# Performance work log

Hardware: AMD Instinct MI355X
Metric: run time of the kernel (lower is better)

Reference implementation:

```python
import jax, jax.numpy as jnp
import numpy as np

EPS_COMBINE = 1e-6   # F.normalize eps in embedder
EPS_FINAL = 1e-12    # F.normalize default eps


def _l2norm(x, eps):
    # torch F.normalize: x / max(||x||_2, eps)
    n = jnp.sqrt(jnp.sum(x * x, axis=-1, keepdims=True))
    return x / jnp.maximum(n, eps)


def setup_inputs() -> dict:
    key = jax.random.key(0)
    ks = jax.random.split(key, 6)
    B, H, E = 16384, 768, 8
    s1 = 1.0 / np.sqrt(H)
    s2 = 1.0 / np.sqrt(H // 2)
    return {
        "embedding": jax.random.normal(ks[0], (B, H), jnp.float32),
        "gate_logits": jax.random.normal(ks[1], (B, E), jnp.float32),
        "W1": jax.random.normal(ks[2], (E, H, H // 2), jnp.float32) * s1,
        "b1": jax.random.normal(ks[3], (E, H // 2), jnp.float32) * s1,
        "W2": jax.random.normal(ks[4], (E, H // 2, H), jnp.float32) * s2,
        "b2": jax.random.normal(ks[5], (E, H), jnp.float32) * s2,
    }


def reference(embedding, gate_logits, W1, b1, W2, b2):
    # cls(): softmax + top-1 mask (sbmoe_top1)
    p = jax.nn.softmax(gate_logits, axis=-1)               # [B, E]
    mask = jax.nn.one_hot(jnp.argmax(p, axis=-1), p.shape[-1], dtype=p.dtype)
    gate = p * mask                                        # [B, E]

    # embedder(): run EVERY expert (2-layer MLP) on all samples
    h = jax.nn.relu(jnp.einsum('bd,edh->beh', embedding, W1) + b1[None])  # [B, E, H/2]
    embs = jnp.einsum('beh,ehd->bed', h, W2) + b2[None]                   # [B, E, H]

    # weighted combine + normalize + residual
    combined = jnp.einsum('bed,be->bd', embs, gate)        # [B, H]
    out = _l2norm(combined, EPS_COMBINE) + embedding
    # normalize=True
    return _l2norm(out, EPS_FINAL)
```

## Files before the change

### kernel.cpp

```cpp
#include <hip/hip_runtime.h>
#include <hip/hip_bf16.h>
#include <stdint.h>

#define B_N   16384
#define H_DIM 768
#define HH    384
#define NE    8
#define CSTRIDE 32

typedef __attribute__((ext_vector_type(8))) short bf16x8;
typedef __attribute__((ext_vector_type(4))) float f32x4;

__device__ __forceinline__ unsigned short f2bf(float f) {
    uint32_t u = __float_as_uint(f);
    return (unsigned short)((u + 0x7fffu + ((u >> 16) & 1u)) >> 16);
}

__global__ void zero_counts_kernel(int* __restrict__ counts) {
    if (threadIdx.x < NE) counts[threadIdx.x * CSTRIDE] = 0;
}

__global__ void route_kernel(const float* __restrict__ logits,
                             int* __restrict__ counts,
                             int* __restrict__ buckets) {
    __shared__ int lcnt[NE];
    __shared__ int lbase[NE];
    const int tid = threadIdx.x;
    if (tid < NE) lcnt[tid] = 0;
    __syncthreads();

    const int b = blockIdx.x * 256 + tid;
    const float* l = logits + (size_t)b * NE;
    float best = l[0];
    int be = 0;
#pragma unroll
    for (int e = 1; e < NE; ++e) {
        float v = l[e];
        if (v > best) { best = v; be = e; }
    }
    const int lpos = atomicAdd(&lcnt[be], 1);
    __syncthreads();
    if (tid < NE) lbase[tid] = atomicAdd(&counts[tid * CSTRIDE], lcnt[tid]);
    __syncthreads();
    buckets[be * B_N + lbase[be] + lpos] = b;
}

__global__ void transpose_cvt_kernel(const float* __restrict__ W1,
                                     const float* __restrict__ W2,
                                     unsigned short* __restrict__ W1T,
                                     unsigned short* __restrict__ W2T,
                                     int* __restrict__ counts) {
    if (blockIdx.x == 0 && blockIdx.y == 0 && blockIdx.z == 0 && threadIdx.x < NE)
        counts[threadIdx.x * CSTRIDE] = 0;

    const int z = blockIdx.z;
    const int R = z ? HH : H_DIM;
    const int C = z ? H_DIM : HH;
    const float* src = (z ? W2 : W1) + (size_t)blockIdx.y * R * C;
    unsigned short* dst = (z ? W2T : W1T) + (size_t)blockIdx.y * R * C;

    const int ctiles = C >> 5;
    const int ty = blockIdx.x / ctiles;
    const int tx = blockIdx.x % ctiles;

    __shared__ float Ts[32][33];
    const int lr = threadIdx.x >> 3;
    const int lc = (threadIdx.x & 7) * 4;

    f32x4 v = *reinterpret_cast<const f32x4*>(src + (size_t)(ty * 32 + lr) * C + tx * 32 + lc);
    Ts[lr][lc + 0] = v[0]; Ts[lr][lc + 1] = v[1];
    Ts[lr][lc + 2] = v[2]; Ts[lr][lc + 3] = v[3];
    __syncthreads();

    ushort4 o;
    o.x = f2bf(Ts[lc + 0][lr]);
    o.y = f2bf(Ts[lc + 1][lr]);
    o.z = f2bf(Ts[lc + 2][lr]);
    o.w = f2bf(Ts[lc + 3][lr]);
    *reinterpret_cast<ushort4*>(dst + (size_t)(tx * 32 + lr) * R + ty * 32 + lc) = o;
}

template<int KTOT, int NTOT, bool A_F32, bool RELU, bool OUTBF>
__global__ __launch_bounds__(512, 6)
void gemm_kernel(const void* __restrict__ Aglob,
                 const unsigned short* __restrict__ WT,
                 const float* __restrict__ bias,
                 const int* __restrict__ counts,
                 const int* __restrict__ buckets,
                 void* __restrict__ Cout) {
    __shared__ __align__(16) unsigned char AsB[2][64 * 128];
    __shared__ __align__(16) unsigned char BsB[2][128 * 128];
    __shared__ int sidx[64];

    const int wgid   = blockIdx.x;
    const int e      = wgid & 7;
    const int rest   = wgid >> 3;
    const int mtile  = rest & 255;
    const int nchunk = rest >> 8;
    const int cnt    = counts[e * CSTRIDE];
    const int base   = mtile * 64;
    if (base >= cnt) return;
    const int ns  = min(64, cnt - base);
    const int tid = threadIdx.x;

    if (tid < 64) sidx[tid] = buckets[e * B_N + base + (tid < ns ? tid : 0)];
    __syncthreads();

    const int ar = tid >> 3, aq = tid & 7;
    const int bn = tid >> 2, bq = tid & 3;
    const float*          arow_f = nullptr;
    const unsigned short* arow_h = nullptr;
    if (A_F32) arow_f = (const float*)Aglob + (size_t)sidx[ar] * KTOT + aq * 8;
    else       arow_h = (const unsigned short*)Aglob + (size_t)sidx[ar] * KTOT + aq * 8;
    const unsigned short* brow =
        WT + ((size_t)e * NTOT + nchunk * 128 + bn) * KTOT + bq * 16;

    const int a_slot  = (ar << 7) + ((aq * 16) ^ ((ar & 7) << 4));
    const int b_slot0 = (bn << 7) + (((bq * 32)     ) ^ ((bn & 7) << 4));
    const int b_slot1 = (bn << 7) + (((bq * 32) + 16) ^ ((bn & 7) << 4));

    const int w = tid >> 6, lane = tid & 63;
    const int wr = w >> 2, wc = w & 3;
    const int fr = lane & 15, fq = lane >> 4;

    f32x4 acc[2][2];
#pragma unroll
    for (int mi = 0; mi < 2; ++mi)
#pragma unroll
        for (int ni = 0; ni < 2; ++ni) acc[mi][ni] = (f32x4)(0.f);

    bf16x8 aReg;
    f32x4  bReg0, bReg1;

    auto LOAD = [&](int k0) {
        if (A_F32) {
            f32x4 f0 = *reinterpret_cast<const f32x4*>(arow_f + k0);
            f32x4 f1 = *reinterpret_cast<const f32x4*>(arow_f + k0 + 4);
            bf16x8 p;
#pragma unroll
            for (int i = 0; i < 4; ++i) {
                p[i]     = (short)f2bf(f0[i]);
                p[i + 4] = (short)f2bf(f1[i]);
            }
            aReg = p;
        } else {
            aReg = *reinterpret_cast<const bf16x8*>(arow_h + k0);
        }
        bReg0 = *reinterpret_cast<const f32x4*>(brow + k0);
        bReg1 = *reinterpret_cast<const f32x4*>(brow + k0 + 8);
    };
    auto WRITE = [&](int buf) {
        *reinterpret_cast<bf16x8*>(&AsB[buf][a_slot])  = aReg;
        *reinterpret_cast<f32x4*>(&BsB[buf][b_slot0]) = bReg0;
        *reinterpret_cast<f32x4*>(&BsB[buf][b_slot1]) = bReg1;
    };
    auto COMPUTE = [&](int buf) {
#pragma unroll
        for (int s = 0; s < 2; ++s) {
            const int kb = s * 64 + fq * 16;
            bf16x8 af[2], bfr[2];
#pragma unroll
            for (int mi = 0; mi < 2; ++mi) {
                int row = wr * 32 + mi * 16 + fr;
                af[mi] = *reinterpret_cast<const bf16x8*>(
                    &AsB[buf][(row << 7) + (kb ^ ((row & 7) << 4))]);
            }
#pragma unroll
            for (int ni = 0; ni < 2; ++ni) {
                int row = wc * 32 + ni * 16 + fr;
                bfr[ni] = *reinterpret_cast<const bf16x8*>(
                    &BsB[buf][(row << 7) + (kb ^ ((row & 7) << 4))]);
            }
#pragma unroll
            for (int mi = 0; mi < 2; ++mi)
#pragma unroll
                for (int ni = 0; ni < 2; ++ni)
                    acc[mi][ni] = __builtin_amdgcn_mfma_f32_16x16x32_bf16(
                        af[mi], bfr[ni], acc[mi][ni], 0, 0, 0);
        }
    };

    LOAD(0);
    WRITE(0);
    __syncthreads();
    int cur = 0;
    for (int k0 = 64; k0 < KTOT; k0 += 64) {
        LOAD(k0);
        COMPUTE(cur);
        WRITE(cur ^ 1);
        __syncthreads();
        cur ^= 1;
    }
    COMPUTE(cur);

    const float* be = bias + (size_t)e * NTOT + nchunk * 128 + wc * 32;
#pragma unroll
    for (int mi = 0; mi < 2; ++mi) {
        const int rl0 = wr * 32 + mi * 16 + fq * 4;
#pragma unroll
        for (int ni = 0; ni < 2; ++ni) {
            const int coll = ni * 16 + fr;
            const int colg = nchunk * 128 + wc * 32 + coll;
            const float bb = be[coll];
#pragma unroll
            for (int r2 = 0; r2 < 4; ++r2) {
                const int rl = rl0 + r2;
                if (rl < ns) {
                    float v = acc[mi][ni][r2] + bb;
                    if (RELU) v = fmaxf(v, 0.f);
                    size_t o = (size_t)sidx[rl] * NTOT + colg;
                    if (OUTBF) ((unsigned short*)Cout)[o] = f2bf(v);
                    else       ((float*)Cout)[o] = v;
                }
            }
        }
    }
}

template<bool YB>
__global__ void norm_kernel(const float* __restrict__ emb,
                            const unsigned short* __restrict__ y2b,
                            float* __restrict__ out) {
    const int row  = blockIdx.x * 4 + (threadIdx.x >> 6);
    const int lane = threadIdx.x & 63;
    const float* x = emb + (size_t)row * H_DIM;
    float* o = out + (size_t)row * H_DIM;

    float s1 = 0.f, s2 = 0.f, s3 = 0.f;
    if (YB) {
        const uint32_t* yrow = reinterpret_cast<const uint32_t*>(y2b + (size_t)row * H_DIM);
        float y0v[6], y1v[6];
        float2 xv[6];
#pragma unroll
        for (int c = 0; c < 6; ++c) {
            uint32_t u = yrow[c * 64 + lane];
            float y0 = __uint_as_float(u << 16);
            float y1 = __uint_as_float(u & 0xffff0000u);
            float2 xx = *reinterpret_cast<const float2*>(x + 2 * (c * 64 + lane));
            y0v[c] = y0; y1v[c] = y1; xv[c] = xx;
            s1 = fmaf(y0, y0, s1); s1 = fmaf(y1, y1, s1);
            s2 = fmaf(y0, xx.x, s2); s2 = fmaf(y1, xx.y, s2);
            s3 = fmaf(xx.x, xx.x, s3); s3 = fmaf(xx.y, xx.y, s3);
        }
#pragma unroll
        for (int m = 1; m < 64; m <<= 1) {
            s1 += __shfl_xor(s1, m); s2 += __shfl_xor(s2, m); s3 += __shfl_xor(s3, m);
        }
        const float n1 = fmaxf(sqrtf(s1), 1e-6f);
        const float i1 = 1.f / n1;
        const float t  = s1 * i1 * i1 + 2.f * s2 * i1 + s3;
        const float i2 = 1.f / fmaxf(sqrtf(t), 1e-12f);
#pragma unroll
        for (int c = 0; c < 6; ++c) {
            float2 ov;
            ov.x = (y0v[c] * i1 + xv[c].x) * i2;
            ov.y = (y1v[c] * i1 + xv[c].y) * i2;
            *reinterpret_cast<float2*>(o + 2 * (c * 64 + lane)) = ov;
        }
    } else {
        f32x4 yv[3], xv[3];
#pragma unroll
        for (int c = 0; c < 3; ++c) {
            int col = c * 256 + lane * 4;
            yv[c] = *reinterpret_cast<const f32x4*>(o + col);
            xv[c] = *reinterpret_cast<const f32x4*>(x + col);
#pragma unroll
            for (int i = 0; i < 4; ++i) {
                s1 = fmaf(yv[c][i], yv[c][i], s1);
                s2 = fmaf(yv[c][i], xv[c][i], s2);
                s3 = fmaf(xv[c][i], xv[c][i], s3);
            }
        }
#pragma unroll
        for (int m = 1; m < 64; m <<= 1) {
            s1 += __shfl_xor(s1, m); s2 += __shfl_xor(s2, m); s3 += __shfl_xor(s3, m);
        }
        const float n1 = fmaxf(sqrtf(s1), 1e-6f);
        const float i1 = 1.f / n1;
        const float t  = s1 * i1 * i1 + 2.f * s2 * i1 + s3;
        const float i2 = 1.f / fmaxf(sqrtf(t), 1e-12f);
#pragma unroll
        for (int c = 0; c < 3; ++c) {
            int col = c * 256 + lane * 4;
            f32x4 ov;
#pragma unroll
            for (int i = 0; i < 4; ++i) ov[i] = (yv[c][i] * i1 + xv[c][i]) * i2;
            *reinterpret_cast<f32x4*>(o + col) = ov;
        }
    }
}

#define TILE 64
#define NTHR 256
#define BK   64
__global__ __launch_bounds__(NTHR, 2)
void moe_fused_fallback(const float* __restrict__ emb,
                        const float* __restrict__ W1,
                        const float* __restrict__ b1,
                        const float* __restrict__ W2,
                        const float* __restrict__ b2,
                        const int* __restrict__ counts,
                        const int* __restrict__ buckets,
                        float* __restrict__ out) {
    __shared__ float Xs[TILE][BK];
    __shared__ __hip_bfloat16 Hs[TILE][HH];
    __shared__ int   sidx[TILE];
    __shared__ float s_in1[TILE];
    __shared__ float s_in2[TILE];

    const int e    = blockIdx.y;
    const int cnt  = counts[e * CSTRIDE];
    const int base = blockIdx.x * TILE;
    if (base >= cnt) return;
    const int ns = min(TILE, cnt - base);
    const int tid = threadIdx.x;
    const int sg  = tid >> 5;
    const int cg  = tid & 31;

    if (tid < TILE) sidx[tid] = buckets[e * B_N + base + ((tid < ns) ? tid : 0)];
    __syncthreads();

    float acc[8][12];
#pragma unroll
    for (int i = 0; i < 8; ++i)
#pragma unroll
        for (int j = 0; j < 12; ++j) acc[i][j] = 0.f;

    const float* W1e = W1 + (size_t)e * H_DIM * HH;
    const int r = tid >> 2, q = tid & 3;
    const float* xrow = emb + (size_t)sidx[r] * H_DIM;

    for (int kk = 0; kk < H_DIM; kk += BK) {
#pragma unroll
        for (int i = 0; i < 4; ++i)
            *reinterpret_cast<float4*>(&Xs[r][q * 16 + i * 4]) =
                *reinterpret_cast<const float4*>(xrow + kk + q * 16 + i * 4);
        __syncthreads();
#pragma unroll 2
        for (int k = 0; k < BK; ++k) {
            float xv[8], wv[12];
            const float* wrow = W1e + (size_t)(kk + k) * HH + cg;
#pragma unroll
            for (int j = 0; j < 12; ++j) wv[j] = wrow[j * 32];
#pragma unroll
            for (int i = 0; i < 8; ++i) xv[i] = Xs[sg * 8 + i][k];
#pragma unroll
            for (int i = 0; i < 8; ++i)
#pragma unroll
                for (int j = 0; j < 12; ++j) acc[i][j] = fmaf(xv[i], wv[j], acc[i][j]);
        }
        __syncthreads();
    }
    const float* b1e = b1 + e * HH;
#pragma unroll
    for (int j = 0; j < 12; ++j) {
        float bb = b1e[cg + j * 32];
#pragma unroll
        for (int i = 0; i < 8; ++i)
            Hs[sg * 8 + i][cg + j * 32] = __float2bfloat16(fmaxf(acc[i][j] + bb, 0.f));
    }
    __syncthreads();

    const float* W2e = W2 + (size_t)e * HH * H_DIM;
    const float* b2e = b2 + e * H_DIM;
    float S1[8], S2[8], S3[8];
#pragma unroll
    for (int i = 0; i < 8; ++i) { S1[i] = 0.f; S2[i] = 0.f; S3[i] = 0.f; }

    for (int hb = 0; hb < H_DIM; hb += 384) {
        float acc2[8][12];
#pragma unroll
        for (int i = 0; i < 8; ++i)
#pragma unroll
            for (int j = 0; j < 12; ++j) acc2[i][j] = 0.f;
#pragma unroll 2
        for (int k = 0; k < HH; ++k) {
            float hv[8], wv[12];
            const float* wrow = W2e + (size_t)k * H_DIM + hb + cg;
#pragma unroll
            for (int j = 0; j < 12; ++j) wv[j] = wrow[j * 32];
#pragma unroll
            for (int i = 0; i < 8; ++i) hv[i] = __bfloat162float(Hs[sg * 8 + i][k]);
#pragma unroll
            for (int i = 0; i < 8; ++i)
#pragma unroll
                for (int j = 0; j < 12; ++j) acc2[i][j] = fmaf(hv[i], wv[j], acc2[i][j]);
        }
#pragma unroll
        for (int j = 0; j < 12; ++j) {
            int col = hb + cg + j * 32;
            float bb = b2e[col];
#pragma unroll
            for (int i = 0; i < 8; ++i) {
                int s = sg * 8 + i;
                float y = acc2[i][j] + bb;
                size_t o = (size_t)sidx[s] * H_DIM + col;
                float x = emb[o];
                S1[i] = fmaf(y, y, S1[i]);
                S2[i] = fmaf(y, x, S2[i]);
                S3[i] = fmaf(x, x, S3[i]);
                if (s < ns) out[o] = y;
            }
        }
    }
#pragma unroll
    for (int i = 0; i < 8; ++i) {
        float v1 = S1[i], v2 = S2[i], v3 = S3[i];
#pragma unroll
        for (int m = 1; m < 32; m <<= 1) {
            v1 += __shfl_xor(v1, m); v2 += __shfl_xor(v2, m); v3 += __shfl_xor(v3, m);
        }
        if (cg == 0) {
            float n1 = fmaxf(sqrtf(v1), 1e-6f);
            float t  = v1 / (n1 * n1) + 2.f * v2 / n1 + v3;
            s_in1[sg * 8 + i] = 1.f / n1;
            s_in2[sg * 8 + i] = 1.f / fmaxf(sqrtf(t), 1e-12f);
        }
    }
    __syncthreads();
#pragma unroll
    for (int i = 0; i < 8; ++i) {
        int s = sg * 8 + i;
        if (s >= ns) continue;
        float in1 = s_in1[s], in2 = s_in2[s];
        size_t rowo = (size_t)sidx[s] * H_DIM;
#pragma unroll
        for (int j = 0; j < 24; ++j) {
            int col = cg + j * 32;
            out[rowo + col] = (out[rowo + col] * in1 + emb[rowo + col]) * in2;
        }
    }
}

extern "C" void kernel_launch(void* const* d_in, const int* in_sizes, int n_in,
                              void* d_out, int out_size, void* d_ws, size_t ws_size,
                              hipStream_t stream) {
    const float* emb    = (const float*)d_in[0];
    const float* logits = (const float*)d_in[1];
    const float* W1     = (const float*)d_in[2];
    const float* b1     = (const float*)d_in[3];
    const float* W2     = (const float*)d_in[4];
    const float* b2     = (const float*)d_in[5];
    float* out = (float*)d_out;

    int* counts  = (int*)d_ws;
    int* buckets = (int*)((char*)d_ws + 1024);
    unsigned short* W1T  = (unsigned short*)((char*)d_ws + 1024 + 524288);
    unsigned short* W2T  = W1T + (size_t)NE * HH * H_DIM;
    unsigned short* Hws  = W2T + (size_t)NE * HH * H_DIM;
    unsigned short* y2ws = Hws + (size_t)B_N * HH;
    const size_t need_base = 1024 + 524288
                           + 2 * (size_t)NE * HH * H_DIM * sizeof(unsigned short)
                           + (size_t)B_N * HH * sizeof(unsigned short);
    const size_t need_bf16 = need_base + (size_t)B_N * H_DIM * sizeof(unsigned short);

    if (ws_size >= need_base) {
        transpose_cvt_kernel<<<dim3(288, NE, 2), 256, 0, stream>>>(W1, W2, W1T, W2T, counts);
        route_kernel<<<B_N / 256, 256, 0, stream>>>(logits, counts, buckets);
        gemm_kernel<H_DIM, HH, true, true, true>
            <<<NE * 256 * 3, 512, 0, stream>>>(emb, W1T, b1, counts, buckets, Hws);
        if (ws_size >= need_bf16) {
            gemm_kernel<HH, H_DIM, false, false, true>
                <<<NE * 256 * 6, 512, 0, stream>>>(Hws, W2T, b2, counts, buckets, y2ws);
            norm_kernel<true><<<B_N / 4, 256, 0, stream>>>(emb, y2ws, out);
        } else {
            gemm_kernel<HH, H_DIM, false, false, false>
                <<<NE * 256 * 6, 512, 0, stream>>>(Hws, W2T, b2, counts, buckets, out);
            norm_kernel<false><<<B_N / 4, 256, 0, stream>>>(emb, nullptr, out);
        }
    } else {
        zero_counts_kernel<<<1, 64, 0, stream>>>(counts);
        route_kernel<<<B_N / 256, 256, 0, stream>>>(logits, counts, buckets);
        moe_fused_fallback<<<dim3(B_N / TILE, NE), NTHR, 0, stream>>>(
            emb, W1, b1, W2, b2, counts, buckets, out);
    }
}
```

Before: 186.2 us.

## Fuse second expert GEMM with L2-normalize and residual epilogue

```diff
diff --git a/kernel.cpp b/kernel.cpp
--- a/kernel.cpp
+++ b/kernel.cpp
@@ -217,75 +217,170 @@
     }
 }
 
-template<bool YB>
-__global__ void norm_kernel(const float* __restrict__ emb,
-                            const unsigned short* __restrict__ y2b,
-                            float* __restrict__ out) {
-    const int row  = blockIdx.x * 4 + (threadIdx.x >> 6);
-    const int lane = threadIdx.x & 63;
-    const float* x = emb + (size_t)row * H_DIM;
-    float* o = out + (size_t)row * H_DIM;
-
-    float s1 = 0.f, s2 = 0.f, s3 = 0.f;
-    if (YB) {
-        const uint32_t* yrow = reinterpret_cast<const uint32_t*>(y2b + (size_t)row * H_DIM);
-        float y0v[6], y1v[6];
-        float2 xv[6];
-#pragma unroll
-        for (int c = 0; c < 6; ++c) {
-            uint32_t u = yrow[c * 64 + lane];
-            float y0 = __uint_as_float(u << 16);
-            float y1 = __uint_as_float(u & 0xffff0000u);
-            float2 xx = *reinterpret_cast<const float2*>(x + 2 * (c * 64 + lane));
-            y0v[c] = y0; y1v[c] = y1; xv[c] = xx;
-            s1 = fmaf(y0, y0, s1); s1 = fmaf(y1, y1, s1);
-            s2 = fmaf(y0, xx.x, s2); s2 = fmaf(y1, xx.y, s2);
-            s3 = fmaf(xx.x, xx.x, s3); s3 = fmaf(xx.y, xx.y, s3);
-        }
-#pragma unroll
-        for (int m = 1; m < 64; m <<= 1) {
-            s1 += __shfl_xor(s1, m); s2 += __shfl_xor(s2, m); s3 += __shfl_xor(s3, m);
-        }
-        const float n1 = fmaxf(sqrtf(s1), 1e-6f);
-        const float i1 = 1.f / n1;
-        const float t  = s1 * i1 * i1 + 2.f * s2 * i1 + s3;
-        const float i2 = 1.f / fmaxf(sqrtf(t), 1e-12f);
-#pragma unroll
-        for (int c = 0; c < 6; ++c) {
-            float2 ov;
-            ov.x = (y0v[c] * i1 + xv[c].x) * i2;
-            ov.y = (y1v[c] * i1 + xv[c].y) * i2;
-            *reinterpret_cast<float2*>(o + 2 * (c * 64 + lane)) = ov;
-        }
-    } else {
-        f32x4 yv[3], xv[3];
-#pragma unroll
-        for (int c = 0; c < 3; ++c) {
-            int col = c * 256 + lane * 4;
-            yv[c] = *reinterpret_cast<const f32x4*>(o + col);
-            xv[c] = *reinterpret_cast<const f32x4*>(x + col);
-#pragma unroll
-            for (int i = 0; i < 4; ++i) {
-                s1 = fmaf(yv[c][i], yv[c][i], s1);
-                s2 = fmaf(yv[c][i], xv[c][i], s2);
-                s3 = fmaf(xv[c][i], xv[c][i], s3);
-            }
-        }
-#pragma unroll
-        for (int m = 1; m < 64; m <<= 1) {
-            s1 += __shfl_xor(s1, m); s2 += __shfl_xor(s2, m); s3 += __shfl_xor(s3, m);
-        }
-        const float n1 = fmaxf(sqrtf(s1), 1e-6f);
-        const float i1 = 1.f / n1;
-        const float t  = s1 * i1 * i1 + 2.f * s2 * i1 + s3;
-        const float i2 = 1.f / fmaxf(sqrtf(t), 1e-12f);
-#pragma unroll
-        for (int c = 0; c < 3; ++c) {
-            int col = c * 256 + lane * 4;
-            f32x4 ov;
-#pragma unroll
-            for (int i = 0; i < 4; ++i) ov[i] = (yv[c][i] * i1 + xv[c][i]) * i2;
-            *reinterpret_cast<f32x4*>(o + col) = ov;
+__global__ __launch_bounds__(512, 2)
+void gemm2n_kernel(const unsigned short* __restrict__ Hws,
+                   const unsigned short* __restrict__ W2T,
+                   const float* __restrict__ b2,
+                   const float* __restrict__ emb,
+                   const int* __restrict__ counts,
+                   const int* __restrict__ buckets,
+                   float* __restrict__ out) {
+    __shared__ __align__(16) unsigned char Adb[2][64 * 64];
+    __shared__ __align__(16) unsigned char Bdb[2][768 * 64];
+    __shared__ int sidx[64];
+    __shared__ float red[3][64][4];
+    __shared__ float inv1s[64], inv2s[64];
+
+    const int wgid  = blockIdx.x;
+    const int e     = wgid & 7;
+    const int mtile = wgid >> 3;
+    const int cnt   = counts[e * CSTRIDE];
+    const int base  = mtile * 64;
+    if (base >= cnt) return;
+    const int ns  = min(64, cnt - base);
+    const int tid = threadIdx.x;
+
+    if (tid < 64) sidx[tid] = buckets[e * B_N + base + (tid < ns ? tid : 0)];
+    __syncthreads();
+
+    const int ar = tid >> 3, aq = tid & 7;
+    const unsigned short* arow = Hws + (size_t)sidx[ar] * HH + aq * 4;
+    const int a_slot = (ar << 6) + ((aq * 8) ^ ((ar & 3) << 4));
+    const unsigned short* Be = W2T + (size_t)e * H_DIM * HH;
+
+    const int w = tid >> 6, lane = tid & 63;
+    const int wr = w >> 2, wc = w & 3;
+    const int fr = lane & 15, fq = lane >> 4;
+
+    f32x4 acc[2][12];
+#pragma unroll
+    for (int mi = 0; mi < 2; ++mi)
+#pragma unroll
+        for (int ni = 0; ni < 12; ++ni) acc[mi][ni] = (f32x4)(0.f);
+
+    float2 aReg;
+    f32x4  bReg0[4], bReg1[4];
+
+    auto LOAD = [&](int k0) {
+        aReg = *reinterpret_cast<const float2*>(arow + k0);
+        const unsigned short* b0 = Be + (size_t)tid * HH + k0;
+#pragma unroll
+        for (int j = 0; j < 4; ++j)
+            bReg0[j] = *reinterpret_cast<const f32x4*>(b0 + j * 8);
+        if (tid < 256) {
+            const unsigned short* b1 = Be + (size_t)(tid + 512) * HH + k0;
+#pragma unroll
+            for (int j = 0; j < 4; ++j)
+                bReg1[j] = *reinterpret_cast<const f32x4*>(b1 + j * 8);
+        }
+    };
+    auto WRITE = [&](int buf) {
+        *reinterpret_cast<float2*>(&Adb[buf][a_slot]) = aReg;
+        const int sw0 = (tid & 3) << 4;
+#pragma unroll
+        for (int j = 0; j < 4; ++j)
+            *reinterpret_cast<f32x4*>(&Bdb[buf][(tid << 6) + ((j * 16) ^ sw0)]) = bReg0[j];
+        if (tid < 256) {
+            const int r2r = tid + 512;
+            const int sw1 = (r2r & 3) << 4;
+#pragma unroll
+            for (int j = 0; j < 4; ++j)
+                *reinterpret_cast<f32x4*>(&Bdb[buf][(r2r << 6) + ((j * 16) ^ sw1)]) = bReg1[j];
+        }
+    };
+    auto COMPUTE = [&](int buf) {
+        bf16x8 af[2];
+#pragma unroll
+        for (int mi = 0; mi < 2; ++mi) {
+            int row = wr * 32 + mi * 16 + fr;
+            af[mi] = *reinterpret_cast<const bf16x8*>(
+                &Adb[buf][(row << 6) + ((fq * 16) ^ ((row & 3) << 4))]);
+        }
+#pragma unroll
+        for (int ni = 0; ni < 12; ++ni) {
+            int row = wc * 192 + ni * 16 + fr;
+            bf16x8 bfr = *reinterpret_cast<const bf16x8*>(
+                &Bdb[buf][(row << 6) + ((fq * 16) ^ ((row & 3) << 4))]);
+            acc[0][ni] = __builtin_amdgcn_mfma_f32_16x16x32_bf16(af[0], bfr, acc[0][ni], 0, 0, 0);
+            acc[1][ni] = __builtin_amdgcn_mfma_f32_16x16x32_bf16(af[1], bfr, acc[1][ni], 0, 0, 0);
+        }
+    };
+
+    LOAD(0);
+    WRITE(0);
+    __syncthreads();
+    int cur = 0;
+    for (int it = 1; it < HH / 32; ++it) {
+        LOAD(it * 32);
+        COMPUTE(cur);
+        WRITE(cur ^ 1);
+        __syncthreads();
+        cur ^= 1;
+    }
+    COMPUTE(cur);
+
+    const float* b2e = b2 + (size_t)e * H_DIM + wc * 192;
+    float bb[12];
+#pragma unroll
+    for (int ni = 0; ni < 12; ++ni) bb[ni] = b2e[ni * 16 + fr];
+
+#pragma unroll
+    for (int mi = 0; mi < 2; ++mi) {
+#pragma unroll
+        for (int r2 = 0; r2 < 4; ++r2) {
+            const int grow = wr * 32 + mi * 16 + fq * 4 + r2;
+            const float* xrow = emb + (size_t)sidx[grow] * H_DIM + wc * 192;
+            float p1 = 0.f, p2 = 0.f, p3 = 0.f;
+#pragma unroll
+            for (int ni = 0; ni < 12; ++ni) {
+                float y = acc[mi][ni][r2] + bb[ni];
+                float x = xrow[ni * 16 + fr];
+                p1 = fmaf(y, y, p1);
+                p2 = fmaf(y, x, p2);
+                p3 = fmaf(x, x, p3);
+            }
+#pragma unroll
+            for (int m = 1; m < 16; m <<= 1) {
+                p1 += __shfl_xor(p1, m);
+                p2 += __shfl_xor(p2, m);
+                p3 += __shfl_xor(p3, m);
+            }
+            if (fr == 0) {
+                red[0][grow][wc] = p1;
+                red[1][grow][wc] = p2;
+                red[2][grow][wc] = p3;
+            }
+        }
+    }
+    __syncthreads();
+    if (tid < 64) {
+        float s1 = red[0][tid][0] + red[0][tid][1] + red[0][tid][2] + red[0][tid][3];
+        float s2 = red[1][tid][0] + red[1][tid][1] + red[1][tid][2] + red[1][tid][3];
+        float s3 = red[2][tid][0] + red[2][tid][1] + red[2][tid][2] + red[2][tid][3];
+        float n1 = fmaxf(sqrtf(s1), 1e-6f);
+        float i1 = 1.f / n1;
+        float t  = s1 * i1 * i1 + 2.f * s2 * i1 + s3;
+        float i2 = 1.f / fmaxf(sqrtf(t), 1e-12f);
+        inv1s[tid] = i1;
+        inv2s[tid] = i2;
+    }
+    __syncthreads();
+#pragma unroll
+    for (int mi = 0; mi < 2; ++mi) {
+#pragma unroll
+        for (int r2 = 0; r2 < 4; ++r2) {
+            const int grow = wr * 32 + mi * 16 + fq * 4 + r2;
+            if (grow >= ns) continue;
+            const float i1 = inv1s[grow], i2 = inv2s[grow];
+            const size_t ro = (size_t)sidx[grow] * H_DIM + wc * 192;
+            const float* xrow = emb + ro;
+            float* orow = out + ro;
+#pragma unroll
+            for (int ni = 0; ni < 12; ++ni) {
+                float y = acc[mi][ni][r2] + bb[ni];
+                float x = xrow[ni * 16 + fr];
+                orow[ni * 16 + fr] = (y * i1 + x) * i2;
+            }
         }
     }
 }
@@ -445,29 +540,19 @@
 
     int* counts  = (int*)d_ws;
     int* buckets = (int*)((char*)d_ws + 1024);
-    unsigned short* W1T  = (unsigned short*)((char*)d_ws + 1024 + 524288);
-    unsigned short* W2T  = W1T + (size_t)NE * HH * H_DIM;
-    unsigned short* Hws  = W2T + (size_t)NE * HH * H_DIM;
-    unsigned short* y2ws = Hws + (size_t)B_N * HH;
-    const size_t need_base = 1024 + 524288
-                           + 2 * (size_t)NE * HH * H_DIM * sizeof(unsigned short)
-                           + (size_t)B_N * HH * sizeof(unsigned short);
-    const size_t need_bf16 = need_base + (size_t)B_N * H_DIM * sizeof(unsigned short);
-
-    if (ws_size >= need_base) {
+    unsigned short* W1T = (unsigned short*)((char*)d_ws + 1024 + 524288);
+    unsigned short* W2T = W1T + (size_t)NE * HH * H_DIM;
+    unsigned short* Hws = W2T + (size_t)NE * HH * H_DIM;
+    const size_t needed = 1024 + 524288
+                        + 2 * (size_t)NE * HH * H_DIM * sizeof(unsigned short)
+                        + (size_t)B_N * HH * sizeof(unsigned short);
+
+    if (ws_size >= needed) {
         transpose_cvt_kernel<<<dim3(288, NE, 2), 256, 0, stream>>>(W1, W2, W1T, W2T, counts);
         route_kernel<<<B_N / 256, 256, 0, stream>>>(logits, counts, buckets);
         gemm_kernel<H_DIM, HH, true, true, true>
             <<<NE * 256 * 3, 512, 0, stream>>>(emb, W1T, b1, counts, buckets, Hws);
-        if (ws_size >= need_bf16) {
-            gemm_kernel<HH, H_DIM, false, false, true>
-                <<<NE * 256 * 6, 512, 0, stream>>>(Hws, W2T, b2, counts, buckets, y2ws);
-            norm_kernel<true><<<B_N / 4, 256, 0, stream>>>(emb, y2ws, out);
-        } else {
-            gemm_kernel<HH, H_DIM, false, false, false>
-                <<<NE * 256 * 6, 512, 0, stream>>>(Hws, W2T, b2, counts, buckets, out);
-            norm_kernel<false><<<B_N / 4, 256, 0, stream>>>(emb, nullptr, out);
-        }
+        gemm2n_kernel<<<NE * 256, 512, 0, stream>>>(Hws, W2T, b2, emb, counts, buckets, out);
     } else {
         zero_counts_kernel<<<1, 64, 0, stream>>>(counts);
         route_kernel<<<B_N / 256, 256, 0, stream>>>(logits, counts, buckets);
```

Measured after the change: 215.9 us. +16.0%, slower.
